# Optimization experiments

Hardware: AMD Instinct MI355X
Metric: run time of the kernel (lower is better)

The kernel has to match this reference:

```python
import jax, jax.numpy as jnp
import numpy as np

B, N_IN, N_OUT, D_IN, D_OUT = 64, 1152, 10, 8, 16

def setup_inputs() -> dict:
    key = jax.random.key(0)
    k1, k2 = jax.random.split(key)
    # inputs: [B, num_in_caps, in_caps_dims[0]=8, in_caps_dims[1]=1]
    inputs = jax.random.normal(k1, (B, N_IN, D_IN, 1), dtype=jnp.float32)
    # transform matrix: prefix_shape + [in0, out0, 1] = [1, N_IN, N_OUT, 8, 16, 1]
    # TF random_uniform_initializer default: U(-0.05, 0.05)
    transform_mat = jax.random.uniform(
        k2, (1, N_IN, N_OUT, D_IN, D_OUT, 1), dtype=jnp.float32,
        minval=-0.05, maxval=0.05)
    return {"inputs": inputs, "transform_mat": transform_mat}

def reference(inputs, transform_mat):
    # Branch: in_caps_dims[1] == out_caps_dims[1] (== 1).
    # Original TF math (broadcast-multiply + reduce_sum over axis -3):
    #   in_pose[b,n,m,i,1,1] * W[1,n,m,i,o,1] summed over i
    # => votes[b,n,m,o,0] = sum_i inputs[b,n,i,0] * W[0,n,m,i,o,0]
    votes = jnp.einsum('bni,nmio->bnmo', inputs[..., 0], transform_mat[0, ..., 0])
    return votes[..., None]  # [B, N_IN, N_OUT, D_OUT, 1]
```

## Files before the change

### kernel.cpp

```cpp
#include <hip/hip_runtime.h>


constexpr int B     = 64;
constexpr int N_IN  = 1152;
constexpr int N_OUT = 10;
constexpr int D_IN  = 8;
constexpr int D_OUT = 16;
constexpr int KB    = 8;
constexpr int NTHREADS = N_IN * N_OUT * (D_OUT / 4) * (B / KB);

__global__ __launch_bounds__(256)
void Transforming_56195352101061_kernel(const float* __restrict__ in,
                                        const float* __restrict__ W,
                                        float* __restrict__ out) {
    int tid = blockIdx.x * blockDim.x + threadIdx.x;
    if (tid >= NTHREADS) return;

    int lin = tid;
    int o4 = lin & 3;       lin >>= 2;
    int m  = lin % N_OUT;   lin /= N_OUT;
    int n  = lin % N_IN;
    int bb = lin / N_IN;

    const float* wbase = W + ((size_t)(n * N_OUT + m) * D_IN) * D_OUT + o4 * 4;
    float4 w[D_IN];
#pragma unroll
    for (int i = 0; i < D_IN; ++i)
        w[i] = *reinterpret_cast<const float4*>(wbase + i * D_OUT);

    const float* ibase = in + ((size_t)(bb * KB) * N_IN + n) * D_IN;
    float4* out4 = reinterpret_cast<float4*>(out);

#pragma unroll
    for (int j = 0; j < KB; ++j) {
        int b = bb * KB + j;
        const float4* iv = reinterpret_cast<const float4*>(
            ibase + (size_t)j * N_IN * D_IN);
        float4 i0 = iv[0];
        float4 i1 = iv[1];
        float ivals[8] = {i0.x, i0.y, i0.z, i0.w, i1.x, i1.y, i1.z, i1.w};

        float4 acc = {0.f, 0.f, 0.f, 0.f};
#pragma unroll
        for (int i = 0; i < D_IN; ++i) {
            acc.x += ivals[i] * w[i].x;
            acc.y += ivals[i] * w[i].y;
            acc.z += ivals[i] * w[i].z;
            acc.w += ivals[i] * w[i].w;
        }

        out4[((size_t)(b * N_IN + n) * N_OUT + m) * 4 + o4] = acc;
    }
}

extern "C" void kernel_launch(void* const* d_in, const int* in_sizes, int n_in,
                              void* d_out, int out_size, void* d_ws, size_t ws_size,
                              hipStream_t stream) {
    const float* in = (const float*)d_in[0];
    const float* W  = (const float*)d_in[1];
    float* out      = (float*)d_out;

    constexpr int BLOCK = 256;
    constexpr int GRID  = (NTHREADS + BLOCK - 1) / BLOCK;
    Transforming_56195352101061_kernel<<<GRID, BLOCK, 0, stream>>>(in, W, out);
}
```

Baseline: 15.68 us.

## Remap block order for XCD-local weight reuse and use nontemporal output stores

Block IDs are remapped so the eight batch groups that share a weight chunk land on the same XCD under round-robin dispatch, which should raise L2 hits on the transform matrix. Output writes use nontemporal stores so the large write-only result does not evict cached inputs. The accumulation is rewritten with ext_vector_type float4 arithmetic. The mapping hardcodes 1408 and 176 for this problem size and assumes the hardware dispatches blocks to XCDs round-robin.

```diff
diff --git a/kernel.cpp b/kernel.cpp
--- a/kernel.cpp
+++ b/kernel.cpp
@@ -1,5 +1,7 @@
 #include <hip/hip_runtime.h>
 
+
+typedef float floatx4 __attribute__((ext_vector_type(4)));
 
 constexpr int B     = 64;
 constexpr int N_IN  = 1152;
@@ -7,49 +9,58 @@
 constexpr int D_IN  = 8;
 constexpr int D_OUT = 16;
 constexpr int KB    = 8;
-constexpr int NTHREADS = N_IN * N_OUT * (D_OUT / 4) * (B / KB);
+constexpr int NCHUNK = N_IN * N_OUT * 4 / 256;
+constexpr int NBLOCKS = NCHUNK * (B / KB);
 
 __global__ __launch_bounds__(256)
 void Transforming_56195352101061_kernel(const float* __restrict__ in,
                                         const float* __restrict__ W,
                                         float* __restrict__ out) {
-    int tid = blockIdx.x * blockDim.x + threadIdx.x;
-    if (tid >= NTHREADS) return;
+    int id = blockIdx.x;
+    int bb, c;
+    if (id < 1408) {
+        int r = id & 7;
+        int t = id >> 3;
+        bb    = t & 7;
+        c     = (t >> 3) * 8 + r;
+    } else {
+        int k = id - 1408;
+        bb    = k >> 2;
+        c     = 176 + (k & 3);
+    }
 
-    int lin = tid;
-    int o4 = lin & 3;       lin >>= 2;
-    int m  = lin % N_OUT;   lin /= N_OUT;
-    int n  = lin % N_IN;
-    int bb = lin / N_IN;
+    int tid = c * 256 + (int)threadIdx.x;
+    int o4  = tid & 3;
+    int lin = tid >> 2;
+    int m   = lin % N_OUT;
+    int n   = lin / N_OUT;
 
     const float* wbase = W + ((size_t)(n * N_OUT + m) * D_IN) * D_OUT + o4 * 4;
-    float4 w[D_IN];
+    floatx4 w[D_IN];
 #pragma unroll
     for (int i = 0; i < D_IN; ++i)
-        w[i] = *reinterpret_cast<const float4*>(wbase + i * D_OUT);
+        w[i] = *reinterpret_cast<const floatx4*>(wbase + i * D_OUT);
 
     const float* ibase = in + ((size_t)(bb * KB) * N_IN + n) * D_IN;
-    float4* out4 = reinterpret_cast<float4*>(out);
+    floatx4* out4 = reinterpret_cast<floatx4*>(out);
 
 #pragma unroll
     for (int j = 0; j < KB; ++j) {
         int b = bb * KB + j;
-        const float4* iv = reinterpret_cast<const float4*>(
+        const floatx4* iv = reinterpret_cast<const floatx4*>(
             ibase + (size_t)j * N_IN * D_IN);
-        float4 i0 = iv[0];
-        float4 i1 = iv[1];
+        floatx4 i0 = iv[0];
+        floatx4 i1 = iv[1];
         float ivals[8] = {i0.x, i0.y, i0.z, i0.w, i1.x, i1.y, i1.z, i1.w};
 
-        float4 acc = {0.f, 0.f, 0.f, 0.f};
+        floatx4 acc = {0.f, 0.f, 0.f, 0.f};
 #pragma unroll
         for (int i = 0; i < D_IN; ++i) {
-            acc.x += ivals[i] * w[i].x;
-            acc.y += ivals[i] * w[i].y;
-            acc.z += ivals[i] * w[i].z;
-            acc.w += ivals[i] * w[i].w;
+            acc += ivals[i] * w[i];
         }
 
-        out4[((size_t)(b * N_IN + n) * N_OUT + m) * 4 + o4] = acc;
+        __builtin_nontemporal_store(acc,
+            &out4[((size_t)(b * N_IN + n) * N_OUT + m) * 4 + o4]);
     }
 }
 
@@ -60,7 +71,5 @@
     const float* W  = (const float*)d_in[1];
     float* out      = (float*)d_out;
 
-    constexpr int BLOCK = 256;
-    constexpr int GRID  = (NTHREADS + BLOCK - 1) / BLOCK;
-    Transforming_56195352101061_kernel<<<GRID, BLOCK, 0, stream>>>(in, W, out);
+    Transforming_56195352101061_kernel<<<NBLOCKS, 256, 0, stream>>>(in, W, out);
 }
```

Result: faster. 14.12 us (-9.9%).
